# Kernel optimization log

Measured on AMD Instinct MI355X. Metric: run time of the kernel, lower is better.

Reference implementation:

```python
import jax, jax.numpy as jnp
import numpy as np

EDGE_THRESHOLD = 0.1
N_NODES, IN_DIM, OUT_DIM, EDGE_DIM = 512, 128, 128, 64
LN_EPS = 1e-5


def setup_inputs() -> dict:
    key = jax.random.key(0)
    ks = jax.random.split(key, 20)
    s = 0.05
    d_in2e = 2 * IN_DIM + EDGE_DIM
    return {
        "node_features": jax.random.normal(ks[0], (N_NODES, IN_DIM), jnp.float32),
        "W": jax.random.normal(ks[1], (N_NODES, N_NODES), jnp.float32),
        "M": jax.random.normal(ks[2], (N_NODES, N_NODES), jnp.float32),
        "edge_features": jax.random.normal(ks[3], (N_NODES, N_NODES, EDGE_DIM), jnp.float32),
        # node_mlp: Linear(in,out) -> ReLU -> Linear(out,out)
        "node_w1": jax.random.normal(ks[4], (IN_DIM, OUT_DIM), jnp.float32) * s,
        "node_b1": jnp.zeros((OUT_DIM,), jnp.float32),
        "node_w2": jax.random.normal(ks[5], (OUT_DIM, OUT_DIM), jnp.float32) * s,
        "node_b2": jnp.zeros((OUT_DIM,), jnp.float32),
        # directed_msg: Linear(2*in+edge_dim,out) -> ReLU -> Linear(out,out)
        "dir_w1": jax.random.normal(ks[6], (d_in2e, OUT_DIM), jnp.float32) * s,
        "dir_b1": jnp.zeros((OUT_DIM,), jnp.float32),
        "dir_w2": jax.random.normal(ks[7], (OUT_DIM, OUT_DIM), jnp.float32) * s,
        "dir_b2": jnp.zeros((OUT_DIM,), jnp.float32),
        # bidirected_msg: Linear(2*in,out) -> ReLU -> Linear(out,out)
        "bi_w1": jax.random.normal(ks[8], (2 * IN_DIM, OUT_DIM), jnp.float32) * s,
        "bi_b1": jnp.zeros((OUT_DIM,), jnp.float32),
        "bi_w2": jax.random.normal(ks[9], (OUT_DIM, OUT_DIM), jnp.float32) * s,
        "bi_b2": jnp.zeros((OUT_DIM,), jnp.float32),
        # LayerNorm(out)
        "ln_g": jnp.ones((OUT_DIM,), jnp.float32),
        "ln_b": jnp.zeros((OUT_DIM,), jnp.float32),
    }


def reference(node_features, W, M, edge_features,
              node_w1, node_b1, node_w2, node_b2,
              dir_w1, dir_b1, dir_w2, dir_b2,
              bi_w1, bi_b1, bi_w2, bi_b2,
              ln_g, ln_b):
    n, d = node_features.shape
    x = node_features

    # self path
    h_self = jax.nn.relu(x @ node_w1 + node_b1) @ node_w2 + node_b2

    # directed messages: msg[j,i] = MLP([x_j, x_i, e_{j,i}]), weight = |W[j,i]| masked.
    # First linear split by concat blocks to avoid materializing (n,n,2d+e).
    src = x @ dir_w1[:d]                 # (n,h)   parent/source term
    tgt = x @ dir_w1[d:2 * d]            # (n,h)   target term
    edg = jnp.einsum('jie,eh->jih', edge_features, dir_w1[2 * d:])  # (n,n,h)
    h1 = jax.nn.relu(src[:, None, :] + tgt[None, :, :] + edg + dir_b1)  # (n,n,h) [j,i]
    msg_d = h1 @ dir_w2 + dir_b2         # (n,n,out)
    absW = jnp.abs(W)
    wd = jnp.where(absW > EDGE_THRESHOLD, absW, 0.0)  # (n,n) [parent j, target i]
    h_dir = jnp.einsum('jio,ji->io', msg_d, wd)

    # bidirected messages: for node i, neighbors j: MLP([x_j, x_i]), weight = |M[i,j]| masked, j != i
    bsrc = x @ bi_w1[:d]
    btgt = x @ bi_w1[d:]
    h1b = jax.nn.relu(bsrc[:, None, :] + btgt[None, :, :] + bi_b1)  # (n,n,h) [j,i]
    msg_b = h1b @ bi_w2 + bi_b2
    absM = jnp.abs(M)
    wb = jnp.where(absM > EDGE_THRESHOLD, absM, 0.0)
    wb = wb * (1.0 - jnp.eye(n, dtype=wb.dtype))  # exclude self
    h_bi = jnp.einsum('jio,ij->io', msg_b, wb)

    h = h_self + h_dir + h_bi
    mu = jnp.mean(h, axis=-1, keepdims=True)
    var = jnp.mean(jnp.square(h - mu), axis=-1, keepdims=True)
    return (h - mu) * jax.lax.rsqrt(var + LN_EPS) * ln_g + ln_b
```

## Files before the change

### kernel.cpp

```cpp
#include <hip/hip_runtime.h>
#include <hip/hip_bf16.h>
#include <cstdint>

#define NN 512
#define DD 128
#define EE 64
#define THR 0.1f
#define NCHUNK 16

typedef __bf16 bf16x8 __attribute__((ext_vector_type(8)));
typedef float  f32x4  __attribute__((ext_vector_type(4)));

__device__ __forceinline__ void stage16(const float* g, float* l) {
    __builtin_amdgcn_global_load_lds(
        (const __attribute__((address_space(1))) uint32_t*)g,
        (__attribute__((address_space(3))) uint32_t*)l, 16, 0, 0);
}

__global__ __launch_bounds__(256) void k_zero(float* __restrict__ p, int n)
{
    int i = blockIdx.x * 256 + threadIdx.x;
    if (i < n) p[i] = 0.f;
}

__global__ __launch_bounds__(128) void k_pre(
    const float* __restrict__ x,
    const float* __restrict__ dw1, const float* __restrict__ bw1,
    const float* __restrict__ nw1, const float* __restrict__ nb1,
    float* __restrict__ src, float* __restrict__ tgt,
    float* __restrict__ bsrc, float* __restrict__ btgt, float* __restrict__ hmid)
{
    const int i0 = blockIdx.x * 4;
    const int h  = threadIdx.x;
    const int which = blockIdx.y;
    const float* B; float* outp;
    switch (which) {
        case 0:  B = dw1;          outp = src;  break;
        case 1:  B = dw1 + DD*DD;  outp = tgt;  break;
        case 2:  B = bw1;          outp = bsrc; break;
        case 3:  B = bw1 + DD*DD;  outp = btgt; break;
        default: B = nw1;          outp = hmid; break;
    }
    __shared__ float sx[4][DD];
    for (int idx = h; idx < 4*DD; idx += DD)
        sx[idx >> 7][idx & 127] = x[i0*DD + idx];
    __syncthreads();
    float a0=0.f, a1=0.f, a2=0.f, a3=0.f;
    for (int k = 0; k < DD; ++k) {
        float w = B[k*DD + h];
        a0 = fmaf(sx[0][k], w, a0);
        a1 = fmaf(sx[1][k], w, a1);
        a2 = fmaf(sx[2][k], w, a2);
        a3 = fmaf(sx[3][k], w, a3);
    }
    if (which == 4) {
        float bb = nb1[h];
        a0 = fmaxf(a0+bb, 0.f); a1 = fmaxf(a1+bb, 0.f);
        a2 = fmaxf(a2+bb, 0.f); a3 = fmaxf(a3+bb, 0.f);
    }
    outp[(i0+0)*DD + h] = a0;
    outp[(i0+1)*DD + h] = a1;
    outp[(i0+2)*DD + h] = a2;
    outp[(i0+3)*DD + h] = a3;
}

__global__ __launch_bounds__(256, 4) void k_msg(
    const float* __restrict__ ef, const float* __restrict__ W,
    const float* __restrict__ M,
    const float* __restrict__ dw1, const float* __restrict__ db1,
    const float* __restrict__ src, const float* __restrict__ tgt,
    const float* __restrict__ bsrc, const float* __restrict__ btgt,
    const float* __restrict__ bb1,
    float* __restrict__ td_base, float* __restrict__ tb_base,
    float* __restrict__ wsum_d, float* __restrict__ wsum_b, int partial)
{
    __shared__ float smem[8704];
    const int bid  = blockIdx.x;
    const int role = bid & 1;
    const int sub  = bid >> 1;
    const int i0    = (sub & 31) * 16;
    const int jbase = (sub >> 5) * 32;
    const int chunk = sub >> 5;
    const int tid   = threadIdx.x;

    if (role == 0) {
        float* stg   = smem;
        float* s_src = smem + 4096;
        float* s_wd  = smem + 8192;
        const int wv   = tid >> 6;
        const int l    = tid & 63;
        const int lrow = l & 15, lhi = l >> 4;

        const int srow = tid >> 4;
        const int sst  = tid & 15;
        const int slog = (sst & 8) | ((sst & 7) ^ (srow & 7));
        const float* gsrc0 = ef + ((size_t)jbase*NN + i0 + srow)*EE + slog*4;
        float* ldst = stg + tid*4;

        #pragma unroll
        for (int t = 0; t < 4; ++t)
            stage16(gsrc0 + (size_t)t*NN*EE, ldst + t*1024);

        for (int idx = tid; idx < 32*DD/4; idx += 256)
            ((float4*)s_src)[idx] = ((const float4*)(src + jbase*DD))[idx];
        for (int idx = tid; idx < 32*16; idx += 256) {
            int jj = idx >> 4, ii = idx & 15;
            float w = fabsf(W[(size_t)(jbase + jj)*NN + i0 + ii]);
            s_wd[idx] = (w > THR) ? w : 0.0f;
        }

        bf16x8 bfrag[2][2];
        #pragma unroll
        for (int nfl = 0; nfl < 2; ++nfl)
            #pragma unroll
            for (int kf = 0; kf < 2; ++kf) {
                bf16x8 t;
                #pragma unroll
                for (int e = 0; e < 8; ++e)
                    t[e] = (__bf16)dw1[(2*DD + kf*32 + lhi*8 + e)*DD + (wv*2+nfl)*16 + lrow];
                bfrag[nfl][kf] = t;
            }
        float tpre[2][4];
        #pragma unroll
        for (int nfl = 0; nfl < 2; ++nfl)
            #pragma unroll
            for (int r = 0; r < 4; ++r) {
                int hh = (wv*2+nfl)*16 + lrow;
                tpre[nfl][r] = tgt[(i0 + lhi*4 + r)*DD + hh] + db1[hh];
            }

        int ro[4];
        #pragma unroll
        for (int h2 = 0; h2 < 2; ++h2)
            #pragma unroll
            for (int q = 0; q < 2; ++q) {
                int slot = h2*8 + lhi*2 + q;
                int st = (slot & 8) | ((slot & 7) ^ (lrow & 7));
                ro[h2*2 + q] = lrow*64 + st*4;
            }

        float acc[2][4] = {};
        __syncthreads();

#define READ_TILE(BUF)                                                        \
        {                                                                     \
            const float* buf_ = (BUF);                                        \
            float4 f0 = *(const float4*)(buf_ + ro[0]);                       \
            float4 f1 = *(const float4*)(buf_ + ro[1]);                       \
            float4 f2 = *(const float4*)(buf_ + ro[2]);                       \
            float4 f3 = *(const float4*)(buf_ + ro[3]);                       \
            af0[0]=(__bf16)f0.x; af0[1]=(__bf16)f0.y;                         \
            af0[2]=(__bf16)f0.z; af0[3]=(__bf16)f0.w;                         \
            af0[4]=(__bf16)f1.x; af0[5]=(__bf16)f1.y;                         \
            af0[6]=(__bf16)f1.z; af0[7]=(__bf16)f1.w;                         \
            af1[0]=(__bf16)f2.x; af1[1]=(__bf16)f2.y;                         \
            af1[2]=(__bf16)f2.z; af1[3]=(__bf16)f2.w;                         \
            af1[4]=(__bf16)f3.x; af1[5]=(__bf16)f3.y;                         \
            af1[6]=(__bf16)f3.z; af1[7]=(__bf16)f3.w;                         \
        }

#define MATH_TILE(T)                                                          \
        {                                                                     \
            float wdv[4];                                                     \
            _Pragma("unroll")                                                 \
            for (int r = 0; r < 4; ++r) wdv[r] = s_wd[(T)*16 + lhi*4 + r];    \
            _Pragma("unroll")                                                 \
            for (int nfl = 0; nfl < 2; ++nfl) {                               \
                f32x4 z = {0.f, 0.f, 0.f, 0.f};                               \
                z = __builtin_amdgcn_mfma_f32_16x16x32_bf16(af0, bfrag[nfl][0], z, 0, 0, 0); \
                z = __builtin_amdgcn_mfma_f32_16x16x32_bf16(af1, bfrag[nfl][1], z, 0, 0, 0); \
                float sv = s_src[(T)*DD + (wv*2+nfl)*16 + lrow];              \
                _Pragma("unroll")                                             \
                for (int r = 0; r < 4; ++r) {                                 \
                    float v = z[r] + sv + tpre[nfl][r];                       \
                    acc[nfl][r] = fmaf(wdv[r], fmaxf(v, 0.f), acc[nfl][r]);   \
                }                                                             \
            }                                                                 \
        }

        bf16x8 af0, af1;
        for (int t = 0; t < 28; ++t) {
            asm volatile("s_waitcnt vmcnt(3)" ::: "memory");
            __builtin_amdgcn_sched_barrier(0);
            __builtin_amdgcn_s_barrier();
            __builtin_amdgcn_sched_barrier(0);
            READ_TILE(stg + (t & 3)*1024);
            __builtin_amdgcn_sched_barrier(0);
            __builtin_amdgcn_s_barrier();
            stage16(gsrc0 + (size_t)(t + 4)*NN*EE, ldst + (t & 3)*1024);
            MATH_TILE(t);
        }
        asm volatile("s_waitcnt vmcnt(0)" ::: "memory");
        __builtin_amdgcn_sched_barrier(0);
        __builtin_amdgcn_s_barrier();
        for (int t = 28; t < 32; ++t) {
            READ_TILE(stg + (t & 3)*1024);
            MATH_TILE(t);
        }
#undef READ_TILE
#undef MATH_TILE

        float* dst = td_base + (partial ? (size_t)chunk * (NN*DD) : 0);
        #pragma unroll
        for (int nfl = 0; nfl < 2; ++nfl)
            #pragma unroll
            for (int r = 0; r < 4; ++r) {
                int o = (i0 + lhi*4 + r)*DD + (wv*2+nfl)*16 + lrow;
                if (partial) dst[o] = acc[nfl][r];
                else         atomicAdd(&dst[o], acc[nfl][r]);
            }
        if (tid < 16) {
            float s = 0.f;
            #pragma unroll
            for (int jj = 0; jj < 32; ++jj) s += s_wd[jj*16 + tid];
            if (partial) wsum_d[chunk * NN + i0 + tid] = s;
            else         atomicAdd(&wsum_d[i0 + tid], s);
        }
    } else {
        float* s_wb = smem;
        float* s_bs = smem + 512;
        const int il = tid >> 4;
        const int hg = tid & 15;

        for (int idx = tid; idx < 16*32; idx += 256) {
            int r = idx >> 5, jj = idx & 31;
            float m = fabsf(M[(size_t)(i0 + r)*NN + jbase + jj]);
            float w = (m > THR) ? m : 0.f;
            if (i0 + r == jbase + jj) w = 0.f;
            s_wb[idx] = w;
        }
        for (int idx = tid; idx < 32*DD; idx += 256)
            s_bs[idx] = bsrc[jbase*DD + idx];
        __syncthreads();

        float bt[8], acc[8] = {};
        #pragma unroll
        for (int r = 0; r < 8; ++r) {
            int hh = hg*8 + r;
            bt[r] = btgt[(i0 + il)*DD + hh] + bb1[hh];
        }
        for (int jj = 0; jj < 32; ++jj) {
            float w = s_wb[il*32 + jj];
            const float* sp = &s_bs[jj*DD + hg*8];
            float4 v0 = *(const float4*)sp;
            float4 v1 = *(const float4*)(sp + 4);
            acc[0] = fmaf(w, fmaxf(v0.x + bt[0], 0.f), acc[0]);
            acc[1] = fmaf(w, fmaxf(v0.y + bt[1], 0.f), acc[1]);
            acc[2] = fmaf(w, fmaxf(v0.z + bt[2], 0.f), acc[2]);
            acc[3] = fmaf(w, fmaxf(v0.w + bt[3], 0.f), acc[3]);
            acc[4] = fmaf(w, fmaxf(v1.x + bt[4], 0.f), acc[4]);
            acc[5] = fmaf(w, fmaxf(v1.y + bt[5], 0.f), acc[5]);
            acc[6] = fmaf(w, fmaxf(v1.z + bt[6], 0.f), acc[6]);
            acc[7] = fmaf(w, fmaxf(v1.w + bt[7], 0.f), acc[7]);
        }
        float* dst = tb_base + (partial ? (size_t)chunk * (NN*DD) : 0);
        #pragma unroll
        for (int r = 0; r < 8; ++r) {
            int o = (i0 + il)*DD + hg*8 + r;
            if (partial) dst[o] = acc[r]; else atomicAdd(&dst[o], acc[r]);
        }
        if (tid < 16) {
            float s = 0.f;
            #pragma unroll
            for (int jj = 0; jj < 32; ++jj) s += s_wb[tid*32 + jj];
            if (partial) wsum_b[chunk * NN + i0 + tid] = s;
            else         atomicAdd(&wsum_b[i0 + tid], s);
        }
    }
}

__global__ __launch_bounds__(256) void k_final(
    const float* __restrict__ hmid, const float* __restrict__ nw2, const float* __restrict__ nb2,
    const float* __restrict__ td,   const float* __restrict__ dw2, const float* __restrict__ db2,
    const float* __restrict__ wsd,
    const float* __restrict__ tb,   const float* __restrict__ bw2, const float* __restrict__ bb2,
    const float* __restrict__ wsb,
    const float* __restrict__ lng,  const float* __restrict__ lnb,
    float* __restrict__ out, int cd, int cb, int wpart)
{
    const int tid = threadIdx.x;
    const int r   = tid >> 7;
    const int h   = tid & 127;
    const int row = blockIdx.x * 2 + r;
    const int o   = row * DD + h;

    __shared__ float sm[2][DD], sd[2][DD], sb[2][DD];
    __shared__ float red[4];

    float vm = hmid[o];
    float s1 = 0.f, s2 = 0.f;
    #pragma unroll 4
    for (int c = 0; c < cd; ++c) s1 += td[(size_t)c*(NN*DD) + o];
    #pragma unroll 4
    for (int c = 0; c < cb; ++c) s2 += tb[(size_t)c*(NN*DD) + o];
    sm[r][h] = vm; sd[r][h] = s1; sb[r][h] = s2;
    __syncthreads();

    float wsum_d_row, wsum_b_row;
    if (wpart) {
        float a = 0.f, b = 0.f;
        #pragma unroll
        for (int c = 0; c < NCHUNK; ++c) {
            a += wsd[c*NN + row];
            b += wsb[c*NN + row];
        }
        wsum_d_row = a; wsum_b_row = b;
    } else {
        wsum_d_row = wsd[row]; wsum_b_row = wsb[row];
    }

    float acc = nb2[h] + wsum_d_row*db2[h] + wsum_b_row*bb2[h];
    #pragma unroll 4
    for (int k = 0; k < DD; ++k) {
        acc += sm[r][k]*nw2[k*DD + h] + sd[r][k]*dw2[k*DD + h] + sb[r][k]*bw2[k*DD + h];
    }

    const int wid = tid >> 6;
    float s = acc;
    #pragma unroll
    for (int off = 32; off > 0; off >>= 1) s += __shfl_down(s, off);
    if ((tid & 63) == 0) red[wid] = s;
    __syncthreads();
    float mu = (red[2*r] + red[2*r + 1]) * (1.0f/128.0f);
    float dv = acc - mu;
    float q  = dv * dv;
    __syncthreads();
    #pragma unroll
    for (int off = 32; off > 0; off >>= 1) q += __shfl_down(q, off);
    if ((tid & 63) == 0) red[wid] = q;
    __syncthreads();
    float var = (red[2*r] + red[2*r + 1]) * (1.0f/128.0f);
    out[o] = dv * rsqrtf(var + 1e-5f) * lng[h] + lnb[h];
}

extern "C" void kernel_launch(void* const* d_in, const int* in_sizes, int n_in,
                              void* d_out, int out_size, void* d_ws, size_t ws_size,
                              hipStream_t stream)
{
    (void)in_sizes; (void)n_in; (void)out_size;
    const float* x   = (const float*)d_in[0];
    const float* W   = (const float*)d_in[1];
    const float* M   = (const float*)d_in[2];
    const float* ef  = (const float*)d_in[3];
    const float* nw1 = (const float*)d_in[4];
    const float* nb1 = (const float*)d_in[5];
    const float* nw2 = (const float*)d_in[6];
    const float* nb2 = (const float*)d_in[7];
    const float* dw1 = (const float*)d_in[8];
    const float* db1 = (const float*)d_in[9];
    const float* dw2 = (const float*)d_in[10];
    const float* db2 = (const float*)d_in[11];
    const float* bw1 = (const float*)d_in[12];
    const float* bb1 = (const float*)d_in[13];
    const float* bw2 = (const float*)d_in[14];
    const float* bb2 = (const float*)d_in[15];
    const float* lng = (const float*)d_in[16];
    const float* lnb = (const float*)d_in[17];
    float* out = (float*)d_out;
    float* ws  = (float*)d_ws;

    const size_t TD = (size_t)NN * DD;
    const size_t WS_PART = (size_t)NCHUNK * NN;
    const size_t PART_FLOATS = 32*TD + 2*WS_PART + 5*TD;
    const int partial = (ws_size >= PART_FLOATS * 4) ? 1 : 0;

    float *t_dir, *t_bi, *wsd, *wsb, *base;
    if (partial) {
        t_dir = ws;
        t_bi  = ws + 16*TD;
        wsd   = ws + 32*TD;
        wsb   = wsd + WS_PART;
        base  = wsb + WS_PART;
    } else {
        t_dir = ws;
        t_bi  = ws + TD;
        wsd   = ws + 2*TD;
        wsb   = wsd + 512;
        base  = ws + 2*TD + 1024;
        int nz = (int)(2*TD + 1024);
        k_zero<<<(nz + 255)/256, 256, 0, stream>>>(ws, nz);
    }
    float* src  = base;
    float* tgt  = base + TD;
    float* bsrc = base + 2*TD;
    float* btgt = base + 3*TD;
    float* hmid = base + 4*TD;

    k_pre  <<<dim3(NN/4, 5), 128, 0, stream>>>(x, dw1, bw1, nw1, nb1,
                                               src, tgt, bsrc, btgt, hmid);
    k_msg  <<<1024, 256, 0, stream>>>(ef, W, M, dw1, db1, src, tgt,
                                      bsrc, btgt, bb1,
                                      t_dir, t_bi, wsd, wsb, partial);
    const int cd = partial ? NCHUNK : 1;
    k_final<<<NN/2, 256, 0, stream>>>(hmid, nw2, nb2, t_dir, dw2, db2, wsd,
                                      t_bi, bw2, bb2, wsb, lng, lnb, out,
                                      cd, cd, partial);
}
```

Before: 54.87 us.

## Deepen edge-feature LDS pipeline to 8 buffers and process two tiles per barrier

The directed-message path of k_msg now stages edge-feature tiles into an 8-slot LDS ring with six tiles in flight, up from four slots. Each loop iteration handles two tiles and needs only one workgroup barrier, down from two per tile. Staging is rescheduled so each phase refills the two slots read in the previous phase. The cost is more LDS per block (about 51 KB), and the launch-bounds occupancy hint drops from 4 to 3 blocks, which may reduce latency hiding across blocks.

```diff
diff --git a/kernel.cpp b/kernel.cpp
--- a/kernel.cpp
+++ b/kernel.cpp
@@ -64,7 +64,7 @@
     outp[(i0+3)*DD + h] = a3;
 }
 
-__global__ __launch_bounds__(256, 4) void k_msg(
+__global__ __launch_bounds__(256, 3) void k_msg(
     const float* __restrict__ ef, const float* __restrict__ W,
     const float* __restrict__ M,
     const float* __restrict__ dw1, const float* __restrict__ db1,
@@ -74,7 +74,7 @@
     float* __restrict__ td_base, float* __restrict__ tb_base,
     float* __restrict__ wsum_d, float* __restrict__ wsum_b, int partial)
 {
-    __shared__ float smem[8704];
+    __shared__ float smem[12800];
     const int bid  = blockIdx.x;
     const int role = bid & 1;
     const int sub  = bid >> 1;
@@ -85,8 +85,8 @@
 
     if (role == 0) {
         float* stg   = smem;
-        float* s_src = smem + 4096;
-        float* s_wd  = smem + 8192;
+        float* s_src = smem + 8192;
+        float* s_wd  = smem + 12288;
         const int wv   = tid >> 6;
         const int l    = tid & 63;
         const int lrow = l & 15, lhi = l >> 4;
@@ -96,10 +96,11 @@
         const int slog = (sst & 8) | ((sst & 7) ^ (srow & 7));
         const float* gsrc0 = ef + ((size_t)jbase*NN + i0 + srow)*EE + slog*4;
         float* ldst = stg + tid*4;
-
-        #pragma unroll
-        for (int t = 0; t < 4; ++t)
-            stage16(gsrc0 + (size_t)t*NN*EE, ldst + t*1024);
+        const size_t jstep = (size_t)NN * EE;
+
+        #pragma unroll
+        for (int t = 0; t < 6; ++t)
+            stage16(gsrc0 + (size_t)t*jstep, ldst + (t & 7)*1024);
 
         for (int idx = tid; idx < 32*DD/4; idx += 256)
             ((float4*)s_src)[idx] = ((const float4*)(src + jbase*DD))[idx];
@@ -140,26 +141,23 @@
             }
 
         float acc[2][4] = {};
-        __syncthreads();
-
-#define READ_TILE(BUF)                                                        \
-        {                                                                     \
-            const float* buf_ = (BUF);                                        \
-            float4 f0 = *(const float4*)(buf_ + ro[0]);                       \
-            float4 f1 = *(const float4*)(buf_ + ro[1]);                       \
-            float4 f2 = *(const float4*)(buf_ + ro[2]);                       \
-            float4 f3 = *(const float4*)(buf_ + ro[3]);                       \
-            af0[0]=(__bf16)f0.x; af0[1]=(__bf16)f0.y;                         \
-            af0[2]=(__bf16)f0.z; af0[3]=(__bf16)f0.w;                         \
-            af0[4]=(__bf16)f1.x; af0[5]=(__bf16)f1.y;                         \
-            af0[6]=(__bf16)f1.z; af0[7]=(__bf16)f1.w;                         \
-            af1[0]=(__bf16)f2.x; af1[1]=(__bf16)f2.y;                         \
-            af1[2]=(__bf16)f2.z; af1[3]=(__bf16)f2.w;                         \
-            af1[4]=(__bf16)f3.x; af1[5]=(__bf16)f3.y;                         \
-            af1[6]=(__bf16)f3.z; af1[7]=(__bf16)f3.w;                         \
-        }
-
-#define MATH_TILE(T)                                                          \
+
+        asm volatile("s_waitcnt lgkmcnt(0)" ::: "memory");
+        __builtin_amdgcn_sched_barrier(0);
+        __builtin_amdgcn_s_barrier();
+        __builtin_amdgcn_sched_barrier(0);
+
+#define CONV(dst0, dst1, f0, f1, f2, f3)                                      \
+        dst0[0]=(__bf16)f0.x; dst0[1]=(__bf16)f0.y;                           \
+        dst0[2]=(__bf16)f0.z; dst0[3]=(__bf16)f0.w;                           \
+        dst0[4]=(__bf16)f1.x; dst0[5]=(__bf16)f1.y;                           \
+        dst0[6]=(__bf16)f1.z; dst0[7]=(__bf16)f1.w;                           \
+        dst1[0]=(__bf16)f2.x; dst1[1]=(__bf16)f2.y;                           \
+        dst1[2]=(__bf16)f2.z; dst1[3]=(__bf16)f2.w;                           \
+        dst1[4]=(__bf16)f3.x; dst1[5]=(__bf16)f3.y;                           \
+        dst1[6]=(__bf16)f3.z; dst1[7]=(__bf16)f3.w;
+
+#define MATH_TILE(T, A0, A1)                                                  \
         {                                                                     \
             float wdv[4];                                                     \
             _Pragma("unroll")                                                 \
@@ -167,8 +165,8 @@
             _Pragma("unroll")                                                 \
             for (int nfl = 0; nfl < 2; ++nfl) {                               \
                 f32x4 z = {0.f, 0.f, 0.f, 0.f};                               \
-                z = __builtin_amdgcn_mfma_f32_16x16x32_bf16(af0, bfrag[nfl][0], z, 0, 0, 0); \
-                z = __builtin_amdgcn_mfma_f32_16x16x32_bf16(af1, bfrag[nfl][1], z, 0, 0, 0); \
+                z = __builtin_amdgcn_mfma_f32_16x16x32_bf16(A0, bfrag[nfl][0], z, 0, 0, 0); \
+                z = __builtin_amdgcn_mfma_f32_16x16x32_bf16(A1, bfrag[nfl][1], z, 0, 0, 0); \
                 float sv = s_src[(T)*DD + (wv*2+nfl)*16 + lrow];              \
                 _Pragma("unroll")                                             \
                 for (int r = 0; r < 4; ++r) {                                 \
@@ -178,26 +176,38 @@
             }                                                                 \
         }
 
-        bf16x8 af0, af1;
-        for (int t = 0; t < 28; ++t) {
-            asm volatile("s_waitcnt vmcnt(3)" ::: "memory");
+        bf16x8 aA0, aA1, aB0, aB1;
+        for (int ph = 0; ph < 16; ++ph) {
+            const int t = ph * 2;
+            if (ph <= 13)      asm volatile("s_waitcnt vmcnt(4)" ::: "memory");
+            else if (ph == 14) asm volatile("s_waitcnt vmcnt(2)" ::: "memory");
+            else               asm volatile("s_waitcnt vmcnt(0)" ::: "memory");
             __builtin_amdgcn_sched_barrier(0);
             __builtin_amdgcn_s_barrier();
             __builtin_amdgcn_sched_barrier(0);
-            READ_TILE(stg + (t & 3)*1024);
-            __builtin_amdgcn_sched_barrier(0);
-            __builtin_amdgcn_s_barrier();
-            stage16(gsrc0 + (size_t)(t + 4)*NN*EE, ldst + (t & 3)*1024);
-            MATH_TILE(t);
-        }
-        asm volatile("s_waitcnt vmcnt(0)" ::: "memory");
-        __builtin_amdgcn_sched_barrier(0);
-        __builtin_amdgcn_s_barrier();
-        for (int t = 28; t < 32; ++t) {
-            READ_TILE(stg + (t & 3)*1024);
-            MATH_TILE(t);
-        }
-#undef READ_TILE
+
+            const float* bufA = stg + ((t    ) & 7)*1024;
+            const float* bufB = stg + ((t + 1) & 7)*1024;
+            float4 fA0 = *(const float4*)(bufA + ro[0]);
+            float4 fA1 = *(const float4*)(bufA + ro[1]);
+            float4 fA2 = *(const float4*)(bufA + ro[2]);
+            float4 fA3 = *(const float4*)(bufA + ro[3]);
+            float4 fB0 = *(const float4*)(bufB + ro[0]);
+            float4 fB1 = *(const float4*)(bufB + ro[1]);
+            float4 fB2 = *(const float4*)(bufB + ro[2]);
+            float4 fB3 = *(const float4*)(bufB + ro[3]);
+
+            if (ph <= 12) {
+                stage16(gsrc0 + (size_t)(t + 6)*jstep, ldst + ((t + 6) & 7)*1024);
+                stage16(gsrc0 + (size_t)(t + 7)*jstep, ldst + ((t + 7) & 7)*1024);
+            }
+
+            CONV(aA0, aA1, fA0, fA1, fA2, fA3)
+            MATH_TILE(t, aA0, aA1)
+            CONV(aB0, aB1, fB0, fB1, fB2, fB3)
+            MATH_TILE(t + 1, aB0, aB1)
+        }
+#undef CONV
 #undef MATH_TILE
 
         float* dst = td_base + (partial ? (size_t)chunk * (NN*DD) : 0);
```

After: 58.22 us. +6.1%, slower.

## Retile directed-message blocks to 64 targets by 8 sources with double-buffered staging

Applied to the files above, without the earlier changes.

Directed-path blocks now cover 64 target nodes and 8 source nodes instead of 16 targets and 32 sources. Each staged j-tile is a 64x64 edge-feature slab, double-buffered with global_load_lds, and the per-wave B fragments and src rows are reused across four row subtiles. The intent is more MFMA work per barrier and fewer barriers per tile. The cost is 64 partial chunks, which makes the final reduction read and the partial workspace four times larger. The bidirected bsrc load is also vectorised to float4.

```diff
diff --git a/kernel.cpp b/kernel.cpp
--- a/kernel.cpp
+++ b/kernel.cpp
@@ -6,7 +6,8 @@
 #define DD 128
 #define EE 64
 #define THR 0.1f
-#define NCHUNK 16
+#define NCH_D 64
+#define NCH_B 16
 
 typedef __bf16 bf16x8 __attribute__((ext_vector_type(8)));
 typedef float  f32x4  __attribute__((ext_vector_type(4)));
@@ -74,38 +75,32 @@
     float* __restrict__ td_base, float* __restrict__ tb_base,
     float* __restrict__ wsum_d, float* __restrict__ wsum_b, int partial)
 {
-    __shared__ float smem[8704];
+    __shared__ float smem[9728];
     const int bid  = blockIdx.x;
     const int role = bid & 1;
     const int sub  = bid >> 1;
-    const int i0    = (sub & 31) * 16;
-    const int jbase = (sub >> 5) * 32;
-    const int chunk = sub >> 5;
-    const int tid   = threadIdx.x;
+    const int tid  = threadIdx.x;
 
     if (role == 0) {
+        const int i0    = (sub & 7) * 64;
+        const int chunk = sub >> 3;
+        const int j0    = chunk * 8;
         float* stg   = smem;
-        float* s_src = smem + 4096;
-        float* s_wd  = smem + 8192;
+        float* s_src = smem + 8192;
+        float* s_wd  = smem + 9216;
         const int wv   = tid >> 6;
         const int l    = tid & 63;
         const int lrow = l & 15, lhi = l >> 4;
 
-        const int srow = tid >> 4;
+        const int trow = tid >> 4;
         const int sst  = tid & 15;
-        const int slog = (sst & 8) | ((sst & 7) ^ (srow & 7));
-        const float* gsrc0 = ef + ((size_t)jbase*NN + i0 + srow)*EE + slog*4;
-        float* ldst = stg + tid*4;
-
-        #pragma unroll
-        for (int t = 0; t < 4; ++t)
-            stage16(gsrc0 + (size_t)t*NN*EE, ldst + t*1024);
-
-        for (int idx = tid; idx < 32*DD/4; idx += 256)
-            ((float4*)s_src)[idx] = ((const float4*)(src + jbase*DD))[idx];
-        for (int idx = tid; idx < 32*16; idx += 256) {
-            int jj = idx >> 4, ii = idx & 15;
-            float w = fabsf(W[(size_t)(jbase + jj)*NN + i0 + ii]);
+        const int slog = (sst & 8) | ((sst & 7) ^ (trow & 7));
+        const float* gstage = ef + ((size_t)(i0 + trow))*EE + (size_t)slog*4;
+
+        ((float4*)s_src)[tid] = ((const float4*)(src + j0*DD))[tid];
+        for (int idx = tid; idx < 8*64; idx += 256) {
+            int jj = idx >> 6, ii = idx & 63;
+            float w = fabsf(W[(size_t)(j0 + jj)*NN + i0 + ii]);
             s_wd[idx] = (w > THR) ? w : 0.0f;
         }
 
@@ -120,103 +115,119 @@
                     t[e] = (__bf16)dw1[(2*DD + kf*32 + lhi*8 + e)*DD + (wv*2+nfl)*16 + lrow];
                 bfrag[nfl][kf] = t;
             }
-        float tpre[2][4];
-        #pragma unroll
-        for (int nfl = 0; nfl < 2; ++nfl)
-            #pragma unroll
-            for (int r = 0; r < 4; ++r) {
-                int hh = (wv*2+nfl)*16 + lrow;
-                tpre[nfl][r] = tgt[(i0 + lhi*4 + r)*DD + hh] + db1[hh];
-            }
+        float tpre[4][2][4];
+        #pragma unroll
+        for (int s = 0; s < 4; ++s)
+            #pragma unroll
+            for (int nfl = 0; nfl < 2; ++nfl)
+                #pragma unroll
+                for (int r = 0; r < 4; ++r) {
+                    int hh = (wv*2+nfl)*16 + lrow;
+                    tpre[s][nfl][r] = tgt[(i0 + s*16 + lhi*4 + r)*DD + hh] + db1[hh];
+                }
 
         int ro[4];
         #pragma unroll
-        for (int h2 = 0; h2 < 2; ++h2)
-            #pragma unroll
-            for (int q = 0; q < 2; ++q) {
-                int slot = h2*8 + lhi*2 + q;
-                int st = (slot & 8) | ((slot & 7) ^ (lrow & 7));
-                ro[h2*2 + q] = lrow*64 + st*4;
-            }
-
-        float acc[2][4] = {};
-        __syncthreads();
-
-#define READ_TILE(BUF)                                                        \
+        for (int kf = 0; kf < 2; ++kf)
+            #pragma unroll
+            for (int q = 0; q < 2; ++q)
+                ro[kf*2 + q] = ((kf*8) | (((lhi*2 + q) ^ (lrow & 7)) & 7)) * 4;
+
+        float acc[4][2][4] = {};
+
+        asm volatile("s_waitcnt vmcnt(0) lgkmcnt(0)" ::: "memory");
+        __builtin_amdgcn_sched_barrier(0);
+
+#define STAGE(J, BUF)                                                         \
         {                                                                     \
-            const float* buf_ = (BUF);                                        \
-            float4 f0 = *(const float4*)(buf_ + ro[0]);                       \
-            float4 f1 = *(const float4*)(buf_ + ro[1]);                       \
-            float4 f2 = *(const float4*)(buf_ + ro[2]);                       \
-            float4 f3 = *(const float4*)(buf_ + ro[3]);                       \
-            af0[0]=(__bf16)f0.x; af0[1]=(__bf16)f0.y;                         \
-            af0[2]=(__bf16)f0.z; af0[3]=(__bf16)f0.w;                         \
-            af0[4]=(__bf16)f1.x; af0[5]=(__bf16)f1.y;                         \
-            af0[6]=(__bf16)f1.z; af0[7]=(__bf16)f1.w;                         \
-            af1[0]=(__bf16)f2.x; af1[1]=(__bf16)f2.y;                         \
-            af1[2]=(__bf16)f2.z; af1[3]=(__bf16)f2.w;                         \
-            af1[4]=(__bf16)f3.x; af1[5]=(__bf16)f3.y;                         \
-            af1[6]=(__bf16)f3.z; af1[7]=(__bf16)f3.w;                         \
-        }
-
-#define MATH_TILE(T)                                                          \
-        {                                                                     \
+            const float* g_ = gstage + (size_t)(j0 + (J))*NN*EE;              \
+            float* l_ = stg + (BUF)*4096 + tid*4;                             \
+            stage16(g_,          l_);                                         \
+            stage16(g_ + 1024,   l_ + 1024);                                  \
+            stage16(g_ + 2048,   l_ + 2048);                                  \
+            stage16(g_ + 3072,   l_ + 3072);                                  \
+        }
+
+        STAGE(0, 0)
+        __builtin_amdgcn_sched_barrier(0);
+        __builtin_amdgcn_s_barrier();
+        __builtin_amdgcn_sched_barrier(0);
+
+#define MATH_TILE(T, BUF)                                                     \
+        _Pragma("unroll")                                                     \
+        for (int s = 0; s < 4; ++s) {                                         \
+            const float* bufs_ = stg + (BUF)*4096 + (s*16 + lrow)*64;         \
+            float4 f00 = *(const float4*)(bufs_ + ro[0]);                     \
+            float4 f01 = *(const float4*)(bufs_ + ro[1]);                     \
+            float4 f10 = *(const float4*)(bufs_ + ro[2]);                     \
+            float4 f11 = *(const float4*)(bufs_ + ro[3]);                     \
+            bf16x8 a0_, a1_;                                                  \
+            a0_[0]=(__bf16)f00.x; a0_[1]=(__bf16)f00.y;                       \
+            a0_[2]=(__bf16)f00.z; a0_[3]=(__bf16)f00.w;                       \
+            a0_[4]=(__bf16)f01.x; a0_[5]=(__bf16)f01.y;                       \
+            a0_[6]=(__bf16)f01.z; a0_[7]=(__bf16)f01.w;                       \
+            a1_[0]=(__bf16)f10.x; a1_[1]=(__bf16)f10.y;                       \
+            a1_[2]=(__bf16)f10.z; a1_[3]=(__bf16)f10.w;                       \
+            a1_[4]=(__bf16)f11.x; a1_[5]=(__bf16)f11.y;                       \
+            a1_[6]=(__bf16)f11.z; a1_[7]=(__bf16)f11.w;                       \
             float wdv[4];                                                     \
             _Pragma("unroll")                                                 \
-            for (int r = 0; r < 4; ++r) wdv[r] = s_wd[(T)*16 + lhi*4 + r];    \
+            for (int r = 0; r < 4; ++r)                                       \
+                wdv[r] = s_wd[(T)*64 + s*16 + lhi*4 + r];                     \
             _Pragma("unroll")                                                 \
             for (int nfl = 0; nfl < 2; ++nfl) {                               \
                 f32x4 z = {0.f, 0.f, 0.f, 0.f};                               \
-                z = __builtin_amdgcn_mfma_f32_16x16x32_bf16(af0, bfrag[nfl][0], z, 0, 0, 0); \
-                z = __builtin_amdgcn_mfma_f32_16x16x32_bf16(af1, bfrag[nfl][1], z, 0, 0, 0); \
+                z = __builtin_amdgcn_mfma_f32_16x16x32_bf16(a0_, bfrag[nfl][0], z, 0, 0, 0); \
+                z = __builtin_amdgcn_mfma_f32_16x16x32_bf16(a1_, bfrag[nfl][1], z, 0, 0, 0); \
                 float sv = s_src[(T)*DD + (wv*2+nfl)*16 + lrow];              \
                 _Pragma("unroll")                                             \
                 for (int r = 0; r < 4; ++r) {                                 \
-                    float v = z[r] + sv + tpre[nfl][r];                       \
-                    acc[nfl][r] = fmaf(wdv[r], fmaxf(v, 0.f), acc[nfl][r]);   \
+                    float v = z[r] + sv + tpre[s][nfl][r];                    \
+                    acc[s][nfl][r] = fmaf(wdv[r], fmaxf(v, 0.f), acc[s][nfl][r]); \
                 }                                                             \
             }                                                                 \
         }
 
-        bf16x8 af0, af1;
-        for (int t = 0; t < 28; ++t) {
-            asm volatile("s_waitcnt vmcnt(3)" ::: "memory");
+        #pragma unroll
+        for (int j = 0; j < 8; ++j) {
+            if (j > 0) {
+                __builtin_amdgcn_sched_barrier(0);
+                __builtin_amdgcn_s_barrier();
+                __builtin_amdgcn_sched_barrier(0);
+            }
+            if (j < 7) STAGE(j + 1, (j + 1) & 1)
+            if (j < 7) asm volatile("s_waitcnt vmcnt(4)" ::: "memory");
+            else       asm volatile("s_waitcnt vmcnt(0)" ::: "memory");
             __builtin_amdgcn_sched_barrier(0);
             __builtin_amdgcn_s_barrier();
             __builtin_amdgcn_sched_barrier(0);
-            READ_TILE(stg + (t & 3)*1024);
-            __builtin_amdgcn_sched_barrier(0);
-            __builtin_amdgcn_s_barrier();
-            stage16(gsrc0 + (size_t)(t + 4)*NN*EE, ldst + (t & 3)*1024);
-            MATH_TILE(t);
-        }
-        asm volatile("s_waitcnt vmcnt(0)" ::: "memory");
-        __builtin_amdgcn_sched_barrier(0);
-        __builtin_amdgcn_s_barrier();
-        for (int t = 28; t < 32; ++t) {
-            READ_TILE(stg + (t & 3)*1024);
-            MATH_TILE(t);
-        }
-#undef READ_TILE
+            MATH_TILE(j, j & 1)
+        }
+#undef STAGE
 #undef MATH_TILE
 
         float* dst = td_base + (partial ? (size_t)chunk * (NN*DD) : 0);
         #pragma unroll
-        for (int nfl = 0; nfl < 2; ++nfl)
-            #pragma unroll
-            for (int r = 0; r < 4; ++r) {
-                int o = (i0 + lhi*4 + r)*DD + (wv*2+nfl)*16 + lrow;
-                if (partial) dst[o] = acc[nfl][r];
-                else         atomicAdd(&dst[o], acc[nfl][r]);
-            }
-        if (tid < 16) {
+        for (int s = 0; s < 4; ++s)
+            #pragma unroll
+            for (int nfl = 0; nfl < 2; ++nfl)
+                #pragma unroll
+                for (int r = 0; r < 4; ++r) {
+                    int o = (i0 + s*16 + lhi*4 + r)*DD + (wv*2+nfl)*16 + lrow;
+                    if (partial) dst[o] = acc[s][nfl][r];
+                    else         atomicAdd(&dst[o], acc[s][nfl][r]);
+                }
+        if (tid < 64) {
             float s = 0.f;
             #pragma unroll
-            for (int jj = 0; jj < 32; ++jj) s += s_wd[jj*16 + tid];
+            for (int jj = 0; jj < 8; ++jj) s += s_wd[jj*64 + tid];
             if (partial) wsum_d[chunk * NN + i0 + tid] = s;
             else         atomicAdd(&wsum_d[i0 + tid], s);
         }
     } else {
+        const int i0    = (sub & 31) * 16;
+        const int jbase = (sub >> 5) * 32;
+        const int chunk = sub >> 5;
         float* s_wb = smem;
         float* s_bs = smem + 512;
         const int il = tid >> 4;
@@ -229,8 +240,8 @@
             if (i0 + r == jbase + jj) w = 0.f;
             s_wb[idx] = w;
         }
-        for (int idx = tid; idx < 32*DD; idx += 256)
-            s_bs[idx] = bsrc[jbase*DD + idx];
+        for (int idx = tid; idx < 32*DD/4; idx += 256)
+            ((float4*)s_bs)[idx] = ((const float4*)(bsrc + jbase*DD))[idx];
         __syncthreads();
 
         float bt[8], acc[8] = {};
@@ -289,7 +300,7 @@
 
     float vm = hmid[o];
     float s1 = 0.f, s2 = 0.f;
-    #pragma unroll 4
+    #pragma unroll 8
     for (int c = 0; c < cd; ++c) s1 += td[(size_t)c*(NN*DD) + o];
     #pragma unroll 4
     for (int c = 0; c < cb; ++c) s2 += tb[(size_t)c*(NN*DD) + o];
@@ -299,11 +310,10 @@
     float wsum_d_row, wsum_b_row;
     if (wpart) {
         float a = 0.f, b = 0.f;
-        #pragma unroll
-        for (int c = 0; c < NCHUNK; ++c) {
-            a += wsd[c*NN + row];
-            b += wsb[c*NN + row];
-        }
+        #pragma unroll 8
+        for (int c = 0; c < cd; ++c) a += wsd[c*NN + row];
+        #pragma unroll 4
+        for (int c = 0; c < cb; ++c) b += wsb[c*NN + row];
         wsum_d_row = a; wsum_b_row = b;
     } else {
         wsum_d_row = wsd[row]; wsum_b_row = wsb[row];
@@ -360,17 +370,18 @@
     float* ws  = (float*)d_ws;
 
     const size_t TD = (size_t)NN * DD;
-    const size_t WS_PART = (size_t)NCHUNK * NN;
-    const size_t PART_FLOATS = 32*TD + 2*WS_PART + 5*TD;
+    const size_t WSD_N = (size_t)NCH_D * NN;
+    const size_t WSB_N = (size_t)NCH_B * NN;
+    const size_t PART_FLOATS = (size_t)(NCH_D + NCH_B)*TD + WSD_N + WSB_N + 5*TD;
     const int partial = (ws_size >= PART_FLOATS * 4) ? 1 : 0;
 
     float *t_dir, *t_bi, *wsd, *wsb, *base;
     if (partial) {
         t_dir = ws;
-        t_bi  = ws + 16*TD;
-        wsd   = ws + 32*TD;
-        wsb   = wsd + WS_PART;
-        base  = wsb + WS_PART;
+        t_bi  = ws + NCH_D*TD;
+        wsd   = t_bi + NCH_B*TD;
+        wsb   = wsd + WSD_N;
+        base  = wsb + WSB_N;
     } else {
         t_dir = ws;
         t_bi  = ws + TD;
@@ -391,8 +402,9 @@
     k_msg  <<<1024, 256, 0, stream>>>(ef, W, M, dw1, db1, src, tgt,
                                       bsrc, btgt, bb1,
                                       t_dir, t_bi, wsd, wsb, partial);
-    const int cd = partial ? NCHUNK : 1;
+    const int cd = partial ? NCH_D : 1;
+    const int cb = partial ? NCH_B : 1;
     k_final<<<NN/2, 256, 0, stream>>>(hmid, nw2, nb2, t_dir, dw2, db2, wsd,
                                       t_bi, bw2, bb2, wsb, lng, lnb, out,
-                                      cd, cd, partial);
-}
+                                      cd, cb, partial);
+}
```

Measured after the change: 209.9 us. +282.6%, slower.
